# Kernel tuning notes

Measured on AMD Instinct MI355X. Metric: run time of the kernel, lower is better.

The kernel has to match this reference:

```python
import jax, jax.numpy as jnp
import numpy as np

N_NODES = 50000


def _add_self_loops(edge_index, n):
    loops = jnp.arange(n, dtype=edge_index.dtype)
    src = jnp.concatenate([edge_index[0], loops])
    dst = jnp.concatenate([edge_index[1], loops])
    return src, dst


def _gcn_norm(src, dst, n):
    # symmetric normalization deg^-1/2 (degrees include self-loops), as in PyG GCNConv
    ones = jnp.ones_like(dst, dtype=jnp.float32)
    deg = jax.ops.segment_sum(ones, dst, num_segments=n)
    dinv = jnp.where(deg > 0, jax.lax.rsqrt(deg), 0.0)
    return dinv[src] * dinv[dst]


def _gcn_conv(x, W, b, src, dst, norm, n):
    h = x @ W                                  # [N, d_out] dense transform first (d_out <= d_in)
    msg = h[src] * norm[:, None]               # gather + per-edge scale
    out = jax.ops.segment_sum(msg, dst, num_segments=n)  # scatter-add aggregation
    return out + b


def setup_inputs() -> dict:
    key = jax.random.key(0)
    ks = jax.random.split(key, 5)
    n, e = N_NODES, 1_600_000
    x = jax.random.normal(ks[0], (n, 512), dtype=jnp.float32)
    edge_index = jax.random.randint(ks[1], (2, e), 0, n, dtype=jnp.int64)
    def glorot(k, fi, fo):
        s = jnp.sqrt(6.0 / (fi + fo)).astype(jnp.float32)
        return jax.random.uniform(k, (fi, fo), jnp.float32, -s, s)
    return {
        "x": x,
        "edge_index": edge_index,
        "W0": glorot(ks[2], 512, 256), "b0": jnp.zeros((256,), jnp.float32),
        "W1": glorot(ks[3], 256, 256), "b1": jnp.zeros((256,), jnp.float32),
        "W2": glorot(ks[4], 256, 128), "b2": jnp.zeros((128,), jnp.float32),
    }


def reference(x, edge_index, W0, b0, W1, b1, W2, b2):
    n = x.shape[0]
    src, dst = _add_self_loops(edge_index, n)
    norm = _gcn_norm(src, dst, n)
    h = jax.nn.relu(_gcn_conv(x, W0, b0, src, dst, norm, n))
    h = jax.nn.relu(_gcn_conv(h, W1, b1, src, dst, norm, n))
    z = _gcn_conv(h, W2, b2, src, dst, norm, n)
    return z
```

## Files before the change

kernel.cpp:

```cpp
#include <hip/hip_runtime.h>
#include <hip/hip_bf16.h>
#include <type_traits>

#define NN 50000

typedef __attribute__((ext_vector_type(8))) short bf16x8;
typedef __attribute__((ext_vector_type(4))) float f32x4;
typedef unsigned int u32;

__device__ __forceinline__ ushort f2bf(float f) {
    unsigned u = __builtin_bit_cast(unsigned, f);
    unsigned r = (u + 0x7fffu + ((u >> 16) & 1u)) >> 16;
    return (ushort)r;
}
__device__ __forceinline__ float bflo(unsigned v) { return __builtin_bit_cast(float, v << 16); }
__device__ __forceinline__ float bfhi(unsigned v) { return __builtin_bit_cast(float, v & 0xffff0000u); }

__device__ __forceinline__ void gld16(const void* g, void* l) {
    __builtin_amdgcn_global_load_lds((const __attribute__((address_space(1))) u32*)g,
                                     (__attribute__((address_space(3))) u32*)l, 16, 0, 0);
}

__global__ void k_init(int* cnt, int* cur, int n, const unsigned int* ei, int npairs, int* flag) {
    int i = blockIdx.x * blockDim.x + threadIdx.x;
    if (i < n) { cnt[i] = 0; cur[i] = 0; }
    if (blockIdx.x == 0) {
        __shared__ int any_nz;
        if (threadIdx.x == 0) any_nz = 0;
        __syncthreads();
        for (int p = threadIdx.x; p < npairs; p += blockDim.x) {
            if (ei[2 * p + 1] != 0u) atomicOr(&any_nz, 1);
        }
        __syncthreads();
        if (threadIdx.x == 0) *flag = (any_nz == 0) ? 1 : 0;
    }
}

__device__ __forceinline__ int load_idx(const void* ei, long long pos, int is64) {
    return is64 ? (int)(((const long long*)ei)[pos]) : ((const int*)ei)[pos];
}

__global__ void k_count(const void* ei, long long E, const int* flag, int* cnt) {
    long long e = (long long)blockIdx.x * blockDim.x + threadIdx.x;
    if (e < E) {
        int dst = load_idx(ei, E + e, *flag);
        atomicAdd(&cnt[dst], 1);
    }
}

__global__ void k_scan(const int* __restrict__ cnt, int* __restrict__ offs,
                       float* __restrict__ dinv, int n) {
    __shared__ int wsum[16];
    __shared__ int carry_s;
    int t = (int)threadIdx.x;
    int lane = t & 63, w = t >> 6;
    if (t == 0) carry_s = 0;
    __syncthreads();
    for (int base = 0; base < n; base += 1024) {
        int i = base + t;
        int v = (i < n) ? cnt[i] : 0;
        int pv = (v + 7) & ~7;
        int x = pv;
#pragma unroll
        for (int off = 1; off < 64; off <<= 1) {
            int y = __shfl_up(x, off);
            if (lane >= off) x += y;
        }
        if (lane == 63) wsum[w] = x;
        __syncthreads();
        if (w == 0) {
            int pvv = (lane < 16) ? wsum[lane] : 0;
#pragma unroll
            for (int off = 1; off < 16; off <<= 1) {
                int py = __shfl_up(pvv, off);
                if (lane >= off) pvv += py;
            }
            if (lane < 16) wsum[lane] = pvv;
        }
        __syncthreads();
        int wbase = (w > 0) ? wsum[w - 1] : 0;
        int incl = x + wbase;
        int excl = incl - pv;
        int carry = carry_s;
        if (i < n) {
            offs[i] = carry + excl;
            dinv[i] = rsqrtf((float)(v + 1));
        }
        __syncthreads();
        if (t == 1023) carry_s = carry + incl;
        __syncthreads();
    }
    if (threadIdx.x == 0) offs[n] = carry_s;
}

__global__ void k_bucket(const void* ei, long long E, const int* __restrict__ flag,
                         const float* __restrict__ dinv, const int* __restrict__ offs,
                         int* cur, int2* __restrict__ epk,
                         const int* __restrict__ cnt, int n) {
    long long e = (long long)blockIdx.x * blockDim.x + threadIdx.x;
    if (e < E) {
        int is64 = *flag;
        int src = load_idx(ei, e, is64);
        int dst = load_idx(ei, E + e, is64);
        int pos = offs[dst] + atomicAdd(&cur[dst], 1);
        epk[pos] = make_int2(src, __builtin_bit_cast(int, dinv[src] * dinv[dst]));
    } else {
        int i = (int)(e - E);
        if (i < n) {
            int b = offs[i] + cnt[i], en = offs[i + 1];
            for (int j = b; j < en; ++j) epk[j] = make_int2(0, 0);
        }
    }
}

__global__ void k_wt3(const float* __restrict__ W0, ushort* __restrict__ WT0,
                      const float* __restrict__ W1, ushort* __restrict__ WT1,
                      const float* __restrict__ W2, ushort* __restrict__ WT2) {
    int id = blockIdx.x * 256 + threadIdx.x;
    const float* W; ushort* WT; int K, N, loc;
    if (id < 131072)      { W = W0; WT = WT0; K = 512; N = 256; loc = id; }
    else if (id < 196608) { W = W1; WT = WT1; K = 256; N = 256; loc = id - 131072; }
    else if (id < 229376) { W = W2; WT = WT2; K = 256; N = 128; loc = id - 196608; }
    else return;
    int nn = loc / K, k = loc - nn * K;
    WT[loc] = f2bf(W[(long long)k * N + nn]);
}

__global__ void k_x2bf(const float* __restrict__ x, ushort* __restrict__ xbf, long long n8) {
    long long id = (long long)blockIdx.x * blockDim.x + threadIdx.x;
    if (id < n8) {
        const float* src = x + id * 8;
        float4 f0 = *(const float4*)src;
        float4 f1 = *(const float4*)(src + 4);
        ushort tmp[8] = {f2bf(f0.x), f2bf(f0.y), f2bf(f0.z), f2bf(f0.w),
                         f2bf(f1.x), f2bf(f1.y), f2bf(f1.z), f2bf(f1.w)};
        *(uint4*)&xbf[id * 8] = *(uint4*)tmp;
    }
}

#define LOFF(r, s) (((r) * 8 + ((s) ^ ((r) & 7))) * 8)

template <typename TA>
__global__ __launch_bounds__(256) void k_gemm_mfma(const TA* __restrict__ A,
                                                   const ushort* __restrict__ WT,
                                                   ushort* __restrict__ C,
                                                   int M, int N, int K) {
    __shared__ ushort As[8192];
    __shared__ ushort Bs[8192];
    int t = threadIdx.x;
    int lane = t & 63;
    int w = t >> 6;
    int wr = (w >> 1) * 64, wc = (w & 1) * 64;
    int m0 = blockIdx.y * 128, n0 = blockIdx.x * 128;

    f32x4 acc[4][4] = {};

    for (int k0 = 0; k0 < K; k0 += 64) {
#pragma unroll
        for (int j = 0; j < 4; ++j) {
            int id = (w * 4 + j) * 64 + lane;
            int r = id >> 3, sp = id & 7;
            int s = sp ^ (r & 7);
            gld16(WT + (long long)(n0 + r) * K + k0 + s * 8, &Bs[(r * 8 + sp) * 8]);
        }
        if constexpr (std::is_same<TA, float>::value) {
#pragma unroll
            for (int j = 0; j < 4; ++j) {
                int id = t + j * 256;
                int r = id >> 3, s = id & 7;
                int grow = m0 + r;
                if (grow < M) {
                    const float* src = A + (long long)grow * K + k0 + s * 8;
                    float4 f0 = *(const float4*)src;
                    float4 f1 = *(const float4*)(src + 4);
                    ushort tmp[8] = {f2bf(f0.x), f2bf(f0.y), f2bf(f0.z), f2bf(f0.w),
                                     f2bf(f1.x), f2bf(f1.y), f2bf(f1.z), f2bf(f1.w)};
                    *(uint4*)&As[LOFF(r, s)] = *(uint4*)tmp;
                }
            }
        } else {
#pragma unroll
            for (int j = 0; j < 4; ++j) {
                int rbase = (w * 4 + j) * 8;
                if (m0 + rbase < M) {
                    int id = rbase * 8 + lane;
                    int r = id >> 3, sp = id & 7;
                    int s = sp ^ (r & 7);
                    gld16((const ushort*)A + (long long)(m0 + r) * K + k0 + s * 8,
                          &As[(r * 8 + sp) * 8]);
                }
            }
        }
        __syncthreads();
#pragma unroll
        for (int kk = 0; kk < 2; ++kk) {
            int ks = kk * 4 + (lane >> 4);
            bf16x8 a[4], b[4];
#pragma unroll
            for (int m = 0; m < 4; ++m)
                a[m] = *(bf16x8*)&As[LOFF(wr + m * 16 + (lane & 15), ks)];
#pragma unroll
            for (int nn = 0; nn < 4; ++nn)
                b[nn] = *(bf16x8*)&Bs[LOFF(wc + nn * 16 + (lane & 15), ks)];
#pragma unroll
            for (int m = 0; m < 4; ++m)
#pragma unroll
                for (int nn = 0; nn < 4; ++nn)
                    acc[m][nn] = __builtin_amdgcn_mfma_f32_16x16x32_bf16(a[m], b[nn], acc[m][nn], 0, 0, 0);
        }
        __syncthreads();
    }
#pragma unroll
    for (int m = 0; m < 4; ++m) {
#pragma unroll
        for (int i = 0; i < 4; ++i) {
            int row = m0 + wr + m * 16 + (lane >> 4) * 4 + i;
            if (row < M) {
#pragma unroll
                for (int nn = 0; nn < 4; ++nn) {
                    int col = n0 + wc + nn * 16 + (lane & 15);
                    C[(long long)row * N + col] = f2bf(acc[m][nn][i]);
                }
            }
        }
    }
}

template <int DT, bool RELU, bool OUTF32>
__global__ __launch_bounds__(128) void k_aggs(const ushort* __restrict__ h,
                                              const int* __restrict__ offs,
                                              const int2* __restrict__ epk,
                                              const float* __restrict__ dinv,
                                              const float* __restrict__ bias,
                                              void* __restrict__ outp, int n, int foff) {
    int node = __builtin_amdgcn_readfirstlane((int)(blockIdx.x * 2 + (threadIdx.x >> 6)));
    if (node >= n) return;
    int t = (int)threadIdx.x & 63;
    float di = dinv[node];
    float dii = di * di;

    unsigned v0 = *(const unsigned*)&h[(long long)node * DT + foff + t * 2];
    float2 bs = *(const float2*)&bias[foff + t * 2];
    float a0 = bs.x + dii * bflo(v0);
    float a1 = bs.y + dii * bfhi(v0);

    int s = offs[node], e = offs[node + 1];

    for (int j = s; j < e; j += 8) {
        int2 p[8];
#pragma unroll
        for (int u = 0; u < 8; ++u) p[u] = epk[j + u];
        unsigned v[8];
#pragma unroll
        for (int u = 0; u < 8; ++u)
            v[u] = *(const unsigned*)&h[(long long)p[u].x * DT + foff + t * 2];
#pragma unroll
        for (int u = 0; u < 8; ++u) {
            float wgt = __builtin_bit_cast(float, p[u].y);
            a0 += wgt * bflo(v[u]);
            a1 += wgt * bfhi(v[u]);
        }
    }

    if (RELU) { a0 = fmaxf(a0, 0.f); a1 = fmaxf(a1, 0.f); }
    long long oidx = ((long long)node * DT + foff) / 2 + t;
    if constexpr (OUTF32) {
        ((float2*)outp)[oidx] = make_float2(a0, a1);
    } else {
        unsigned pk = (unsigned)f2bf(a0) | ((unsigned)f2bf(a1) << 16);
        ((unsigned*)outp)[oidx] = pk;
    }
}

extern "C" void kernel_launch(void* const* d_in, const int* in_sizes, int n_in,
                              void* d_out, int out_size, void* d_ws, size_t ws_size,
                              hipStream_t stream) {
    const float* x  = (const float*)d_in[0];
    const void*  ei = d_in[1];
    const float* W0 = (const float*)d_in[2];
    const float* b0 = (const float*)d_in[3];
    const float* W1 = (const float*)d_in[4];
    const float* b1 = (const float*)d_in[5];
    const float* W2 = (const float*)d_in[6];
    const float* b2 = (const float*)d_in[7];
    float* out = (float*)d_out;

    const int n = NN;
    const long long E = (long long)in_sizes[1] / 2;

    char* ws = (char*)d_ws;
    int*    cnt  = (int*)(ws);
    int*    cur  = (int*)(ws + 256 * 1024);
    int*    offs = (int*)(ws + 512 * 1024);
    float*  dinv = (float*)(ws + 768 * 1024);
    int*    flag = (int*)(ws + 1000 * 1024);
    int2*   epk  = (int2*)(ws + 1024 * 1024);
    ushort* WT0  = (ushort*)(ws + 17ll * 1024 * 1024);
    ushort* WT1  = (ushort*)(ws + 17ll * 1024 * 1024 + 512 * 1024);
    ushort* WT2  = (ushort*)(ws + 17ll * 1024 * 1024 + 768 * 1024);
    ushort* hA   = (ushort*)(ws + 18ll * 1024 * 1024);
    ushort* hB   = (ushort*)(ws + 44ll * 1024 * 1024);
    ushort* xbf  = (ushort*)(ws + 70ll * 1024 * 1024);
    const size_t need_xbf = 70ll * 1024 * 1024 + 51200000ll;

    k_init<<<(n + 255) / 256, 256, 0, stream>>>(cnt, cur, n, (const unsigned int*)ei, 4096, flag);
    k_count<<<(int)((E + 255) / 256), 256, 0, stream>>>(ei, E, flag, cnt);
    k_scan<<<1, 1024, 0, stream>>>(cnt, offs, dinv, n);
    k_bucket<<<(int)((E + n + 255) / 256), 256, 0, stream>>>(ei, E, flag, dinv, offs, cur, epk, cnt, n);

    k_wt3<<<(229376 + 255) / 256, 256, 0, stream>>>(W0, WT0, W1, WT1, W2, WT2);

    int mt = (n + 127) / 128;
    int nb2 = (n + 1) / 2;

    if (ws_size >= need_xbf) {
        long long n8 = (long long)n * 512 / 8;
        k_x2bf<<<(int)((n8 + 255) / 256), 256, 0, stream>>>(x, xbf, n8);
        k_gemm_mfma<ushort><<<dim3(2, mt), 256, 0, stream>>>(xbf, WT0, hA, n, 256, 512);
    } else {
        k_gemm_mfma<float><<<dim3(2, mt), 256, 0, stream>>>(x, WT0, hA, n, 256, 512);
    }
    k_aggs<256, true, false><<<nb2, 128, 0, stream>>>(hA, offs, epk, dinv, b0, hB, n, 0);
    k_aggs<256, true, false><<<nb2, 128, 0, stream>>>(hA, offs, epk, dinv, b0, hB, n, 128);

    k_gemm_mfma<ushort><<<dim3(2, mt), 256, 0, stream>>>(hB, WT1, hA, n, 256, 256);
    k_aggs<256, true, false><<<nb2, 128, 0, stream>>>(hA, offs, epk, dinv, b1, hB, n, 0);
    k_aggs<256, true, false><<<nb2, 128, 0, stream>>>(hA, offs, epk, dinv, b1, hB, n, 128);

    k_gemm_mfma<ushort><<<dim3(1, mt), 256, 0, stream>>>(hB, WT2, hA, n, 128, 256);
    k_aggs<128, false, true><<<nb2, 128, 0, stream>>>(hA, offs, epk, dinv, b2, out, n, 0);
}
```

Baseline: 526.5 us.

## Record per-edge slot in count pass and partition bucket scatter by destination range

The count kernel now stores the atomicAdd return value as each edge's slot within its destination bucket, which removes the second atomic pass and the cur array in the bucket kernel. The bucket kernel is split into 8 destination-range partitions, with blockIdx low bits selecting the partition. Each block scans a chunk of 2048 edges and writes only edges whose destination falls in its range, so scattered writes stay in a smaller region of epk. The cost is reading the dst indices 8 times and the extra ord array, which is stored in the hA buffer before hA is overwritten.

```diff
diff --git a/kernel.cpp b/kernel.cpp
--- a/kernel.cpp
+++ b/kernel.cpp
@@ -21,9 +21,9 @@
                                      (__attribute__((address_space(3))) u32*)l, 16, 0, 0);
 }
 
-__global__ void k_init(int* cnt, int* cur, int n, const unsigned int* ei, int npairs, int* flag) {
+__global__ void k_init(int* cnt, int n, const unsigned int* ei, int npairs, int* flag) {
     int i = blockIdx.x * blockDim.x + threadIdx.x;
-    if (i < n) { cnt[i] = 0; cur[i] = 0; }
+    if (i < n) cnt[i] = 0;
     if (blockIdx.x == 0) {
         __shared__ int any_nz;
         if (threadIdx.x == 0) any_nz = 0;
@@ -40,11 +40,12 @@
     return is64 ? (int)(((const long long*)ei)[pos]) : ((const int*)ei)[pos];
 }
 
-__global__ void k_count(const void* ei, long long E, const int* flag, int* cnt) {
+__global__ void k_count(const void* ei, long long E, const int* flag,
+                        int* cnt, int* __restrict__ ord) {
     long long e = (long long)blockIdx.x * blockDim.x + threadIdx.x;
     if (e < E) {
         int dst = load_idx(ei, E + e, *flag);
-        atomicAdd(&cnt[dst], 1);
+        ord[e] = atomicAdd(&cnt[dst], 1);
     }
 }
 
@@ -93,20 +94,33 @@
     if (threadIdx.x == 0) offs[n] = carry_s;
 }
 
+#define KE 8
 __global__ void k_bucket(const void* ei, long long E, const int* __restrict__ flag,
                          const float* __restrict__ dinv, const int* __restrict__ offs,
-                         int* cur, int2* __restrict__ epk,
-                         const int* __restrict__ cnt, int n) {
-    long long e = (long long)blockIdx.x * blockDim.x + threadIdx.x;
-    if (e < E) {
+                         const int* __restrict__ ord, int2* __restrict__ epk,
+                         const int* __restrict__ cnt, int n, int nchunk_e, int pn) {
+    int p = blockIdx.x & 7;
+    int c = blockIdx.x >> 3;
+    int lo = p * pn;
+    int hi = lo + pn; if (hi > n) hi = n;
+    if (c < nchunk_e) {
         int is64 = *flag;
-        int src = load_idx(ei, e, is64);
-        int dst = load_idx(ei, E + e, is64);
-        int pos = offs[dst] + atomicAdd(&cur[dst], 1);
-        epk[pos] = make_int2(src, __builtin_bit_cast(int, dinv[src] * dinv[dst]));
+        long long base = (long long)c * (256 * KE) + threadIdx.x;
+#pragma unroll
+        for (int k = 0; k < KE; ++k) {
+            long long e = base + k * 256;
+            if (e < E) {
+                int dst = load_idx(ei, E + e, is64);
+                if (dst >= lo && dst < hi) {
+                    int src = load_idx(ei, e, is64);
+                    int pos = offs[dst] + ord[e];
+                    epk[pos] = make_int2(src, __builtin_bit_cast(int, dinv[src] * dinv[dst]));
+                }
+            }
+        }
     } else {
-        int i = (int)(e - E);
-        if (i < n) {
+        int i = lo + (c - nchunk_e) * 256 + (int)threadIdx.x;
+        if (i < hi) {
             int b = offs[i] + cnt[i], en = offs[i + 1];
             for (int j = b; j < en; ++j) epk[j] = make_int2(0, 0);
         }
@@ -290,7 +304,6 @@
 
     char* ws = (char*)d_ws;
     int*    cnt  = (int*)(ws);
-    int*    cur  = (int*)(ws + 256 * 1024);
     int*    offs = (int*)(ws + 512 * 1024);
     float*  dinv = (float*)(ws + 768 * 1024);
     int*    flag = (int*)(ws + 1000 * 1024);
@@ -301,12 +314,19 @@
     ushort* hA   = (ushort*)(ws + 18ll * 1024 * 1024);
     ushort* hB   = (ushort*)(ws + 44ll * 1024 * 1024);
     ushort* xbf  = (ushort*)(ws + 70ll * 1024 * 1024);
+    int*    ord  = (int*)hA;
     const size_t need_xbf = 70ll * 1024 * 1024 + 51200000ll;
 
-    k_init<<<(n + 255) / 256, 256, 0, stream>>>(cnt, cur, n, (const unsigned int*)ei, 4096, flag);
-    k_count<<<(int)((E + 255) / 256), 256, 0, stream>>>(ei, E, flag, cnt);
+    k_init<<<(n + 255) / 256, 256, 0, stream>>>(cnt, n, (const unsigned int*)ei, 4096, flag);
+    k_count<<<(int)((E + 255) / 256), 256, 0, stream>>>(ei, E, flag, cnt, ord);
     k_scan<<<1, 1024, 0, stream>>>(cnt, offs, dinv, n);
-    k_bucket<<<(int)((E + n + 255) / 256), 256, 0, stream>>>(ei, E, flag, dinv, offs, cur, epk, cnt, n);
+    {
+        int nchunk_e = (int)((E + 256 * KE - 1) / (256 * KE));
+        int pn = (n + 7) / 8;
+        int nchunk_pad = (pn + 255) / 256;
+        k_bucket<<<8 * (nchunk_e + nchunk_pad), 256, 0, stream>>>(
+            ei, E, flag, dinv, offs, ord, epk, cnt, n, nchunk_e, pn);
+    }
 
     k_wt3<<<(229376 + 255) / 256, 256, 0, stream>>>(W0, WT0, W1, WT1, W2, WT2);
 
```

New measurement: 514.5 us. 2.3% less time.
